# Performance work log

Hardware: AMD Instinct MI355X
Metric: run time of the kernel (lower is better)

## Reference

```python
import jax, jax.numpy as jnp
import numpy as np

B, T, D, H = 8, 512, 768, 768
LN_EPS = 1e-3  # keras LayerNormalization default epsilon


def setup_inputs() -> dict:
    key = jax.random.key(0)
    ks = jax.random.split(key, 16)
    s = 1.0 / np.sqrt(D)  # glorot-ish scale for weight matrices
    return {
        'x': jax.random.normal(ks[0], (B, T, D), jnp.float32),
        'ln1_g': jnp.ones((D,), jnp.float32),
        'ln1_b': jnp.zeros((D,), jnp.float32),
        'ln2_g': jnp.ones((D,), jnp.float32),
        'ln2_b': jnp.zeros((D,), jnp.float32),
        'tm_mix_k': jax.random.uniform(ks[1], (D,), jnp.float32, 0.0, 2.0 / D),
        'tm_mix_v': jax.random.uniform(ks[2], (D,), jnp.float32, 0.0, 2.0 / D),
        'tm_mix_r': jax.random.uniform(ks[3], (D,), jnp.float32, 0.0, (2.0 / D) ** 0.5),
        'tm_key_w': jax.random.normal(ks[4], (D, H), jnp.float32) * s,
        'tm_value_w': jax.random.normal(ks[5], (D, H), jnp.float32) * s,
        'tm_rec_w': jax.random.normal(ks[6], (D, H), jnp.float32) * s,
        'time_decay': jax.random.uniform(ks[7], (H,), jnp.float32, 0.0, 1.0),
        'time_first': jax.random.uniform(ks[8], (H,), jnp.float32, 0.0, 0.05),
        'out_w': jax.random.normal(ks[9], (H, D), jnp.float32) * s,
        'cm_mix_k': jax.random.uniform(ks[10], (D,), jnp.float32, 0.0, 2.0 / D),
        'cm_mix_r': jax.random.uniform(ks[11], (D,), jnp.float32, 0.0, 2.0 / D),
        'cm_key_w': jax.random.normal(ks[12], (D, 4 * H), jnp.float32) * s,
        'cm_value_w': jax.random.normal(ks[13], (4 * H, D), jnp.float32) * (0.5 * s),
        'cm_rec_w': jax.random.normal(ks[14], (D, D), jnp.float32) * s,
    }


def _layernorm(z, g, b):
    m = jnp.mean(z, axis=-1, keepdims=True)
    v = jnp.var(z, axis=-1, keepdims=True)
    return (z - m) * jax.lax.rsqrt(v + LN_EPS) * g + b


def reference(x, ln1_g, ln1_b, ln2_g, ln2_b, tm_mix_k, tm_mix_v, tm_mix_r,
              tm_key_w, tm_value_w, tm_rec_w, time_decay, time_first, out_w,
              cm_mix_k, cm_mix_r, cm_key_w, cm_value_w, cm_rec_w):
    # x: [B, T, D]. Sequential RWKV WKV recurrence over T via lax.scan.
    def step(carry, x_t):
        s_cm, s_tm, num, den, q = carry  # [B,D],[B,D],[B,H],[B,H],[B,H]
        # ---- time mixing on ln_1(x_t) ----
        xi = _layernorm(x_t, ln1_g, ln1_b)
        xk = xi * tm_mix_k + s_tm * (1.0 - tm_mix_k)
        xv = xi * tm_mix_v + s_tm * (1.0 - tm_mix_v)
        xr = xi * tm_mix_r + s_tm * (1.0 - tm_mix_r)
        k = xk @ tm_key_w                      # [B,H]
        v = xv @ tm_value_w                    # [B,H]
        sr = jax.nn.sigmoid(xr @ tm_rec_w)     # [B,H]
        # max-stabilized wkv readout
        w = time_first + k
        qq = jnp.maximum(q, w)
        e1 = jnp.exp(q - qq)
        e2 = jnp.exp(w - qq)
        wkv = (e1 * num + e2 * v) / (e1 * den + e2)
        # state update with decay
        w2 = q - jnp.exp(time_decay)
        q_new = jnp.maximum(w2, k)
        e1 = jnp.exp(w2 - q_new)
        e2 = jnp.exp(k - q_new)
        num_new = e1 * num + e2 * v
        den_new = e1 * den + e2
        y = x_t + (sr * wkv) @ out_w
        # ---- channel mixing on ln_2(y) ----
        xc = _layernorm(y, ln2_g, ln2_b)
        xk2 = xc * cm_mix_k + s_cm * (1.0 - cm_mix_k)
        xr2 = xc * cm_mix_r + s_cm * (1.0 - cm_mix_r)
        kv = jnp.square(jax.nn.relu(xk2 @ cm_key_w)) @ cm_value_w
        y = y + jax.nn.sigmoid(xr2 @ cm_rec_w) * kv
        return (xc, xi, num_new, den_new, q_new), y

    b = x.shape[0]
    d = tm_key_w.shape[0]
    h = tm_key_w.shape[1]
    zD = jnp.zeros((b, d), x.dtype)
    zH = jnp.zeros((b, h), x.dtype)
    init = (zD, zD, zH, zH, zH)
    _, ys = jax.lax.scan(step, init, jnp.swapaxes(x, 0, 1))  # ys: [T,B,D]
    return jnp.swapaxes(ys, 0, 1)
```

## Files before the change

### kernel.cpp

```cpp
#include <hip/hip_runtime.h>
#include <cstdint>
#include <cstddef>

#define B_ 8
#define T_ 512
#define D_ 768
#define H_ 768
#define BT_ 4096
#define LN_EPS 1e-3f

typedef short bf16x8 __attribute__((ext_vector_type(8)));
typedef float f32x4 __attribute__((ext_vector_type(4)));

__device__ __forceinline__ ushort f2bf(float f) {
    union { float f; unsigned u; } x; x.f = f;
    unsigned r = (x.u + 0x7FFFu + ((x.u >> 16) & 1u)) >> 16;
    return (ushort)r;
}
__device__ __forceinline__ float bf2f(ushort u) {
    union { unsigned u; float f; } x; x.u = ((unsigned)u) << 16;
    return x.f;
}

#define GLOAD_LDS16(gp, lp)                                                        \
    __builtin_amdgcn_global_load_lds((const __attribute__((address_space(1))) void*)(gp), \
                                     (__attribute__((address_space(3))) void*)(lp), 16, 0, 0)

struct PrepArgs {
    const float *x, *g, *b, *mk, *mv, *mr;
    ushort *xk, *xv, *xr;
    const float* ws[7];
    ushort* wd[7];
};

__global__ __launch_bounds__(256) void prep(PrepArgs a) {
    __shared__ float tl[32][33];
    __shared__ float red[4][4];
    int bid = blockIdx.x;
    const int tid = threadIdx.x;
    if (bid < BT_) {
        const int row = bid;
        const int t = row & (T_ - 1);
        const float* xc = a.x + (size_t)row * D_;
        const float* xp = a.x + (size_t)(row - 1) * D_;
        const float c0 = xc[tid], c1 = xc[tid + 256], c2 = xc[tid + 512];
        float p0 = 0.f, p1 = 0.f, p2 = 0.f;
        if (t > 0) { p0 = xp[tid]; p1 = xp[tid + 256]; p2 = xp[tid + 512]; }
        float sc = c0 + c1 + c2, qc = c0 * c0 + c1 * c1 + c2 * c2;
        float sp = p0 + p1 + p2, qp = p0 * p0 + p1 * p1 + p2 * p2;
        #pragma unroll
        for (int off = 32; off > 0; off >>= 1) {
            sc += __shfl_down(sc, off); qc += __shfl_down(qc, off);
            sp += __shfl_down(sp, off); qp += __shfl_down(qp, off);
        }
        const int wid = tid >> 6;
        if ((tid & 63) == 0) { red[wid][0] = sc; red[wid][1] = qc; red[wid][2] = sp; red[wid][3] = qp; }
        __syncthreads();
        sc = red[0][0] + red[1][0] + red[2][0] + red[3][0];
        qc = red[0][1] + red[1][1] + red[2][1] + red[3][1];
        sp = red[0][2] + red[1][2] + red[2][2] + red[3][2];
        qp = red[0][3] + red[1][3] + red[2][3] + red[3][3];
        const float mc = sc * (1.0f / D_);
        const float rc = rsqrtf(qc * (1.0f / D_) - mc * mc + LN_EPS);
        const float mp = sp * (1.0f / D_);
        const float rp = rsqrtf(qp * (1.0f / D_) - mp * mp + LN_EPS);
        const size_t base = (size_t)row * D_;
        const float cv[3] = {c0, c1, c2};
        const float pv[3] = {p0, p1, p2};
        #pragma unroll
        for (int s = 0; s < 3; ++s) {
            const int d = tid + s * 256;
            const float cn = (cv[s] - mc) * rc * a.g[d] + a.b[d];
            const float pn = (t > 0) ? ((pv[s] - mp) * rp * a.g[d] + a.b[d]) : 0.0f;
            float m;
            m = a.mk[d]; a.xk[base + d] = f2bf(cn * m + pn * (1.f - m));
            m = a.mv[d]; a.xv[base + d] = f2bf(cn * m + pn * (1.f - m));
            m = a.mr[d]; a.xr[base + d] = f2bf(cn * m + pn * (1.f - m));
        }
        return;
    }
    bid -= BT_;
    int z, K, N, n0, k0;
    if (bid < 2880) {
        z = bid / 576; const int i = bid % 576;
        K = 768; N = 768; n0 = (i % 24) * 32; k0 = (i / 24) * 32;
    } else if (bid < 2880 + 2304) {
        z = 5; const int i = bid - 2880;
        K = 768; N = 3072; n0 = (i % 96) * 32; k0 = (i / 96) * 32;
    } else {
        z = 6; const int i = bid - 2880 - 2304;
        K = 3072; N = 768; n0 = (i % 24) * 32; k0 = (i / 24) * 32;
    }
    const float* W = a.ws[z];
    ushort* WT = a.wd[z];
    const int tx = tid & 31, ty = tid >> 5;
    #pragma unroll
    for (int i = 0; i < 4; ++i)
        tl[ty + i * 8][tx] = W[(size_t)(k0 + ty + i * 8) * N + n0 + tx];
    __syncthreads();
    #pragma unroll
    for (int i = 0; i < 4; ++i)
        WT[(size_t)(n0 + ty + i * 8) * K + k0 + tx] = f2bf(tl[tx][ty + i * 8]);
}

__global__ __launch_bounds__(256) void ln_cmix(const float* __restrict__ in,
                                               ushort* __restrict__ xk2,
                                               ushort* __restrict__ xr2,
                                               const float* __restrict__ g,
                                               const float* __restrict__ b,
                                               const float* __restrict__ mk,
                                               const float* __restrict__ mr) {
    const int row = blockIdx.x;
    const int t = row & (T_ - 1);
    const float* xc = in + (size_t)row * D_;
    const float* xp = in + (size_t)(row - 1) * D_;
    const int tid = threadIdx.x;
    const float c0 = xc[tid], c1 = xc[tid + 256], c2 = xc[tid + 512];
    float p0 = 0.f, p1 = 0.f, p2 = 0.f;
    if (t > 0) { p0 = xp[tid]; p1 = xp[tid + 256]; p2 = xp[tid + 512]; }
    float sc = c0 + c1 + c2, qc = c0 * c0 + c1 * c1 + c2 * c2;
    float sp = p0 + p1 + p2, qp = p0 * p0 + p1 * p1 + p2 * p2;
    #pragma unroll
    for (int off = 32; off > 0; off >>= 1) {
        sc += __shfl_down(sc, off); qc += __shfl_down(qc, off);
        sp += __shfl_down(sp, off); qp += __shfl_down(qp, off);
    }
    __shared__ float red[4][4];
    const int wid = tid >> 6;
    if ((tid & 63) == 0) { red[wid][0] = sc; red[wid][1] = qc; red[wid][2] = sp; red[wid][3] = qp; }
    __syncthreads();
    sc = red[0][0] + red[1][0] + red[2][0] + red[3][0];
    qc = red[0][1] + red[1][1] + red[2][1] + red[3][1];
    sp = red[0][2] + red[1][2] + red[2][2] + red[3][2];
    qp = red[0][3] + red[1][3] + red[2][3] + red[3][3];
    const float mc = sc * (1.0f / D_);
    const float rc = rsqrtf(qc * (1.0f / D_) - mc * mc + LN_EPS);
    const float mp = sp * (1.0f / D_);
    const float rp = rsqrtf(qp * (1.0f / D_) - mp * mp + LN_EPS);
    const size_t base = (size_t)row * D_;
    const float cv[3] = {c0, c1, c2};
    const float pv[3] = {p0, p1, p2};
    #pragma unroll
    for (int s = 0; s < 3; ++s) {
        const int d = tid + s * 256;
        const float cn = (cv[s] - mc) * rc * g[d] + b[d];
        const float pn = (t > 0) ? ((pv[s] - mp) * rp * g[d] + b[d]) : 0.0f;
        float m;
        m = mk[d]; xk2[base + d] = f2bf(cn * m + pn * (1.f - m));
        m = mr[d]; xr2[base + d] = f2bf(cn * m + pn * (1.f - m));
    }
}

#define WKV_CH 16
#define WKV_NC 16
#define WKV_L  32

__global__ __launch_bounds__(256) void wkv_scan(const ushort* __restrict__ k,
                                                const ushort* __restrict__ v,
                                                const ushort* __restrict__ srr,
                                                const float* __restrict__ time_decay,
                                                const float* __restrict__ time_first,
                                                ushort* __restrict__ rv) {
    const int c   = threadIdx.x & (WKV_CH - 1);
    const int ch  = threadIdx.x >> 4;
    const int gch = blockIdx.x * WKV_CH + c;
    const int b = gch / H_;
    const int h = gch % H_;
    const float ed = expf(time_decay[h]);
    const float tf = time_first[h];
    const size_t base = (size_t)b * T_ * H_ + h;

    float n = 0.f, d = 0.f, m = -1e30f;
    size_t idx = base + (size_t)(ch * WKV_L) * H_;
    #pragma unroll 4
    for (int t = 0; t < WKV_L; ++t, idx += H_) {
        const float kk = bf2f(k[idx]), vv = bf2f(v[idx]);
        const float w2 = m - ed;
        const float qn = fmaxf(w2, kk);
        const float e1 = expf(w2 - qn), e2 = expf(kk - qn);
        n = e1 * n + e2 * vv;
        d = e1 * d + e2;
        m = qn;
    }

    __shared__ float sn[WKV_NC][WKV_CH], sd[WKV_NC][WKV_CH], sm[WKV_NC][WKV_CH];
    sn[ch][c] = n; sd[ch][c] = d; sm[ch][c] = m;
    __syncthreads();

    if (ch == 0) {
        float pn = 0.f, pd = 0.f, pm = -1e30f;
        #pragma unroll
        for (int j = 0; j < WKV_NC; ++j) {
            const float nn = sn[j][c], dd = sd[j][c], m2 = sm[j][c];
            sn[j][c] = pn; sd[j][c] = pd; sm[j][c] = pm;
            const float w2 = pm - ed * (float)WKV_L;
            const float mm = fmaxf(w2, m2);
            const float e1 = expf(w2 - mm), e2 = expf(m2 - mm);
            pn = e1 * pn + e2 * nn;
            pd = e1 * pd + e2 * dd;
            pm = mm;
        }
    }
    __syncthreads();

    n = sn[ch][c]; d = sd[ch][c]; m = sm[ch][c];
    idx = base + (size_t)(ch * WKV_L) * H_;
    #pragma unroll 4
    for (int t = 0; t < WKV_L; ++t, idx += H_) {
        const float kk = bf2f(k[idx]), vv = bf2f(v[idx]), ss = bf2f(srr[idx]);
        const float w  = tf + kk;
        const float qq = fmaxf(m, w);
        const float e1 = expf(m - qq), e2 = expf(w - qq);
        const float wkvv = (e1 * n + e2 * vv) / (e1 * d + e2);
        rv[idx] = f2bf(ss * wkvv);
        const float w2 = m - ed;
        const float qn = fmaxf(w2, kk);
        const float a  = expf(w2 - qn), bb = expf(kk - qn);
        n = a * n + bb * vv;
        d = a * d + bb;
        m = qn;
    }
}

template <int BM, int NF>
__device__ __forceinline__ void run_gemm(const ushort* __restrict__ A,
                                         const ushort* __restrict__ Bt,
                                         int K, int bm, int bn,
                                         ushort* As, ushort* Bs,
                                         f32x4 (&acc)[BM / 32][NF], int t) {
    constexpr int MF = BM / 32;
    constexpr int BN = NF * 32;
    constexpr int ASTRIDE = BM * 64;
    constexpr int BSTRIDE = BN * 64;
    const int l = t & 63, wid = t >> 6;
    const int wr = wid >> 1, wc = wid & 1;
    const int lr = l & 15, lg = l >> 4;
    const int l8 = l >> 3, j8 = l & 7;
    const int gcol = ((j8 ^ l8) << 3);
    const int rsw = lr & 7;

    auto STAGE = [&](int buf, int k0) {
        #pragma unroll
        for (int p = 0; p < MF; ++p) {
            const int r = wid * (BM / 4) + p * 8 + l8;
            GLOAD_LDS16(A + (size_t)(bm + r) * K + k0 + gcol,
                        As + buf * ASTRIDE + (wid * (BM / 4) + p * 8) * 64);
        }
        #pragma unroll
        for (int p = 0; p < NF; ++p) {
            const int r = wid * (BN / 4) + p * 8 + l8;
            GLOAD_LDS16(Bt + (size_t)(bn + r) * K + k0 + gcol,
                        Bs + buf * BSTRIDE + (wid * (BN / 4) + p * 8) * 64);
        }
    };

    STAGE(0, 0);
    const int nt = K >> 6;
    int cur = 0;
    for (int it = 0; it < nt; ++it) {
        if (it + 1 < nt) {
            STAGE(cur ^ 1, (it + 1) << 6);
            constexpr int VC = MF + NF;
            if constexpr (VC == 4)      asm volatile("s_waitcnt vmcnt(4)" ::: "memory");
            else if constexpr (VC == 5) asm volatile("s_waitcnt vmcnt(5)" ::: "memory");
            else if constexpr (VC == 6) asm volatile("s_waitcnt vmcnt(6)" ::: "memory");
            else                        asm volatile("s_waitcnt vmcnt(8)" ::: "memory");
        } else {
            asm volatile("s_waitcnt vmcnt(0)" ::: "memory");
        }
        __builtin_amdgcn_sched_barrier(0);
        __builtin_amdgcn_s_barrier();
        const ushort* Ab = As + cur * ASTRIDE;
        const ushort* Bb = Bs + cur * BSTRIDE;
        #pragma unroll
        for (int ks = 0; ks < 2; ++ks) {
            const int cidx = ((ks * 4 + lg) ^ rsw) << 3;
            bf16x8 af[MF], bfr[NF];
            #pragma unroll
            for (int mf = 0; mf < MF; ++mf)
                af[mf] = *(const bf16x8*)(Ab + (wr * (BM / 2) + mf * 16 + lr) * 64 + cidx);
            #pragma unroll
            for (int nf = 0; nf < NF; ++nf)
                bfr[nf] = *(const bf16x8*)(Bb + (wc * (BN / 2) + nf * 16 + lr) * 64 + cidx);
            #pragma unroll
            for (int mf = 0; mf < MF; ++mf)
                #pragma unroll
                for (int nf = 0; nf < NF; ++nf)
                    acc[mf][nf] = __builtin_amdgcn_mfma_f32_16x16x32_bf16(
                        af[mf], bfr[nf], acc[mf][nf], 0, 0, 0);
        }
        __builtin_amdgcn_s_barrier();
        cur ^= 1;
    }
}

template <int BM, int NF>
__device__ __forceinline__ void run_gemm3(const ushort* __restrict__ A,
                                          const ushort* __restrict__ Bt,
                                          int K, int bm, int bn,
                                          ushort* As, ushort* Bs,
                                          f32x4 (&acc)[BM / 32][NF], int t) {
    constexpr int MF = BM / 32;
    constexpr int BN = NF * 32;
    constexpr int ASTRIDE = BM * 64;
    constexpr int BSTRIDE = BN * 64;
    const int l = t & 63, wid = t >> 6;
    const int wr = wid >> 1, wc = wid & 1;
    const int lr = l & 15, lg = l >> 4;
    const int l8 = l >> 3, j8 = l & 7;
    const int gcol = ((j8 ^ l8) << 3);
    const int rsw = lr & 7;

    auto STAGE = [&](int buf, int k0) {
        #pragma unroll
        for (int p = 0; p < MF; ++p) {
            GLOAD_LDS16(A + (size_t)(bm + wid * (BM / 4) + p * 8 + l8) * K + k0 + gcol,
                        As + buf * ASTRIDE + (wid * (BM / 4) + p * 8) * 64);
        }
        #pragma unroll
        for (int p = 0; p < NF; ++p) {
            GLOAD_LDS16(Bt + (size_t)(bn + wid * (BN / 4) + p * 8 + l8) * K + k0 + gcol,
                        Bs + buf * BSTRIDE + (wid * (BN / 4) + p * 8) * 64);
        }
    };

    const int nt = K >> 6;
    STAGE(0, 0);
    STAGE(1, 64);
    int cur = 0;
    for (int it = 0; it < nt; ++it) {
        if (it + 2 < nt) {
            int nb = cur + 2; if (nb >= 3) nb -= 3;
            STAGE(nb, (it + 2) << 6);
            constexpr int VC2 = 2 * (MF + NF);
            if constexpr (VC2 == 8)       asm volatile("s_waitcnt vmcnt(8)" ::: "memory");
            else if constexpr (VC2 == 12) asm volatile("s_waitcnt vmcnt(12)" ::: "memory");
            else                          asm volatile("s_waitcnt vmcnt(16)" ::: "memory");
        } else if (it + 1 < nt) {
            constexpr int VC = MF + NF;
            if constexpr (VC == 4)      asm volatile("s_waitcnt vmcnt(4)" ::: "memory");
            else if constexpr (VC == 6) asm volatile("s_waitcnt vmcnt(6)" ::: "memory");
            else                        asm volatile("s_waitcnt vmcnt(8)" ::: "memory");
        } else {
            asm volatile("s_waitcnt vmcnt(0)" ::: "memory");
        }
        __builtin_amdgcn_sched_barrier(0);
        __builtin_amdgcn_s_barrier();
        const ushort* Ab = As + cur * ASTRIDE;
        const ushort* Bb = Bs + cur * BSTRIDE;
        #pragma unroll
        for (int ks = 0; ks < 2; ++ks) {
            const int cidx = ((ks * 4 + lg) ^ rsw) << 3;
            bf16x8 af[MF], bfr[NF];
            #pragma unroll
            for (int mf = 0; mf < MF; ++mf)
                af[mf] = *(const bf16x8*)(Ab + (wr * (BM / 2) + mf * 16 + lr) * 64 + cidx);
            #pragma unroll
            for (int nf = 0; nf < NF; ++nf)
                bfr[nf] = *(const bf16x8*)(Bb + (wc * (BN / 2) + nf * 16 + lr) * 64 + cidx);
            #pragma unroll
            for (int mf = 0; mf < MF; ++mf)
                #pragma unroll
                for (int nf = 0; nf < NF; ++nf)
                    acc[mf][nf] = __builtin_amdgcn_mfma_f32_16x16x32_bf16(
                        af[mf], bfr[nf], acc[mf][nf], 0, 0, 0);
        }
        __builtin_amdgcn_s_barrier();
        cur += 1; if (cur >= 3) cur -= 3;
    }
}

enum { EPI_KVR = 0, EPI_ADDX = 1, EPI_RELU2 = 2 };

template <int EPI, int BM, int BN>
__global__ __launch_bounds__(256) void hgemm(const ushort* __restrict__ Abase,
                                             const ushort* __restrict__ Wbase,
                                             void* __restrict__ Cbase,
                                             const float* __restrict__ aux1,
                                             int M, int N, int K) {
    constexpr int NF = BN / 32;
    constexpr int MF = BM / 32;
    __shared__ ushort As[2 * BM * 64];
    __shared__ ushort Bs[2 * BN * 64];
    const int t = threadIdx.x;
    int lin = blockIdx.y * gridDim.x + blockIdx.x;
    const int q = (gridDim.x * gridDim.y) >> 3;
    lin = (lin & 7) * q + (lin >> 3);
    const int bn = (lin % gridDim.x) * BN;
    const int bm = (lin / gridDim.x) * BM;
    const int z = blockIdx.z;

    const ushort* A  = Abase;
    const ushort* Bt = Wbase;
    float*  Cf = (float*)Cbase;
    ushort* Cu = (ushort*)Cbase;
    if (EPI == EPI_KVR) {
        A  += (size_t)z * ((size_t)M * K);
        Bt += (size_t)z * ((size_t)N * K);
        Cu += (size_t)z * ((size_t)M * N);
    }

    f32x4 acc[MF][NF];
    #pragma unroll
    for (int i = 0; i < MF; ++i)
        #pragma unroll
        for (int j = 0; j < NF; ++j) acc[i][j] = (f32x4){0.f, 0.f, 0.f, 0.f};

    run_gemm<BM, NF>(A, Bt, K, bm, bn, As, Bs, acc, t);

    const int l = t & 63, wid = t >> 6;
    const int wr = wid >> 1, wc = wid & 1;
    const int lr = l & 15, lg = l >> 4;
    #pragma unroll
    for (int mf = 0; mf < MF; ++mf) {
        #pragma unroll
        for (int nf = 0; nf < NF; ++nf) {
            const f32x4 a = acc[mf][nf];
            #pragma unroll
            for (int j = 0; j < 4; ++j) {
                const int row = bm + wr * (BM / 2) + mf * 16 + lg * 4 + j;
                const int col = bn + wc * (BN / 2) + nf * 16 + lr;
                const size_t idx = (size_t)row * N + col;
                const float vacc = a[j];
                if (EPI == EPI_KVR) {
                    Cu[idx] = f2bf((z == 2) ? 1.0f / (1.0f + expf(-vacc)) : vacc);
                } else if (EPI == EPI_ADDX) {
                    Cf[idx] = aux1[idx] + vacc;
                } else {
                    const float r = fmaxf(vacc, 0.0f);
                    Cu[idx] = f2bf(r * r);
                }
            }
        }
    }
}

__global__ __launch_bounds__(256) void kv_sigmul(const ushort* __restrict__ h1,
                                                 const ushort* __restrict__ wtCV,
                                                 const ushort* __restrict__ xr2,
                                                 const ushort* __restrict__ wtCR,
                                                 const float* __restrict__ ymid,
                                                 float* __restrict__ out) {
    __shared__ ushort As[3 * 64 * 64];
    __shared__ ushort Bs[3 * 64 * 64];
    const int t = threadIdx.x;
    int lin = blockIdx.y * gridDim.x + blockIdx.x;
    const int q = (gridDim.x * gridDim.y) >> 3;
    lin = (lin & 7) * q + (lin >> 3);
    const int bn = (lin % gridDim.x) * 64;
    const int bm = (lin / gridDim.x) * 64;

    f32x4 acc1[2][2], acc2[2][2];
    #pragma unroll
    for (int i = 0; i < 2; ++i)
        #pragma unroll
        for (int j = 0; j < 2; ++j) {
            acc1[i][j] = (f32x4){0.f, 0.f, 0.f, 0.f};
            acc2[i][j] = (f32x4){0.f, 0.f, 0.f, 0.f};
        }

    run_gemm3<64, 2>(h1, wtCV, 3072, bm, bn, As, Bs, acc1, t);
    run_gemm3<64, 2>(xr2, wtCR, 768, bm, bn, As, Bs, acc2, t);

    const int l = t & 63, wid = t >> 6;
    const int wr = wid >> 1, wc = wid & 1;
    const int lr = l & 15, lg = l >> 4;
    #pragma unroll
    for (int mf = 0; mf < 2; ++mf) {
        #pragma unroll
        for (int nf = 0; nf < 2; ++nf) {
            #pragma unroll
            for (int j = 0; j < 4; ++j) {
                const int row = bm + wr * 32 + mf * 16 + lg * 4 + j;
                const int col = bn + wc * 32 + nf * 16 + lr;
                const size_t idx = (size_t)row * D_ + col;
                const float sig = 1.0f / (1.0f + expf(-acc2[mf][nf][j]));
                out[idx] = ymid[idx] + sig * acc1[mf][nf][j];
            }
        }
    }
}

extern "C" void kernel_launch(void* const* d_in, const int* in_sizes, int n_in,
                              void* d_out, int out_size, void* d_ws, size_t ws_size,
                              hipStream_t stream) {
    const float* x          = (const float*)d_in[0];
    const float* ln1_g      = (const float*)d_in[1];
    const float* ln1_b      = (const float*)d_in[2];
    const float* ln2_g      = (const float*)d_in[3];
    const float* ln2_b      = (const float*)d_in[4];
    const float* tm_mix_k   = (const float*)d_in[5];
    const float* tm_mix_v   = (const float*)d_in[6];
    const float* tm_mix_r   = (const float*)d_in[7];
    const float* tm_key_w   = (const float*)d_in[8];
    const float* tm_value_w = (const float*)d_in[9];
    const float* tm_rec_w   = (const float*)d_in[10];
    const float* time_decay = (const float*)d_in[11];
    const float* time_first = (const float*)d_in[12];
    const float* out_w      = (const float*)d_in[13];
    const float* cm_mix_k   = (const float*)d_in[14];
    const float* cm_mix_r   = (const float*)d_in[15];
    const float* cm_key_w   = (const float*)d_in[16];
    const float* cm_value_w = (const float*)d_in[17];
    const float* cm_rec_w   = (const float*)d_in[18];
    float* out = (float*)d_out;

    const size_t SZ = (size_t)BT_ * D_;
    float* wsf = (float*)d_ws;
    float* ymid = wsf;
    ushort* ub = (ushort*)(wsf + SZ);
    ushort* a0 = ub;
    ushort* a1 = ub + SZ;
    ushort* a2 = ub + 2 * SZ;
    ushort* h1 = ub + 3 * SZ;
    ushort* kvsr = ub + 7 * SZ;
    ushort* wt = ub + 10 * SZ;
    const size_t W66  = (size_t)768 * 768;
    const size_t WBIG = (size_t)768 * 3072;
    ushort* wtK  = wt;
    ushort* wtV  = wt + W66;
    ushort* wtR  = wt + 2 * W66;
    ushort* wtO  = wt + 3 * W66;
    ushort* wtCR = wt + 4 * W66;
    ushort* wtCK = wt + 5 * W66;
    ushort* wtCV = wt + 5 * W66 + WBIG;

    PrepArgs pa;
    pa.x = x; pa.g = ln1_g; pa.b = ln1_b;
    pa.mk = tm_mix_k; pa.mv = tm_mix_v; pa.mr = tm_mix_r;
    pa.xk = a0; pa.xv = a1; pa.xr = a2;
    pa.ws[0] = tm_key_w;   pa.wd[0] = wtK;
    pa.ws[1] = tm_value_w; pa.wd[1] = wtV;
    pa.ws[2] = tm_rec_w;   pa.wd[2] = wtR;
    pa.ws[3] = out_w;      pa.wd[3] = wtO;
    pa.ws[4] = cm_rec_w;   pa.wd[4] = wtCR;
    pa.ws[5] = cm_key_w;   pa.wd[5] = wtCK;
    pa.ws[6] = cm_value_w; pa.wd[6] = wtCV;

    prep<<<BT_ + 2880 + 2304 + 2304, 256, 0, stream>>>(pa);
    hgemm<EPI_KVR, 64, 64><<<dim3(12, 64, 3), 256, 0, stream>>>(a0, wtK, kvsr, nullptr, BT_, 768, 768);
    wkv_scan<<<(B_ * H_) / WKV_CH, 256, 0, stream>>>(kvsr, kvsr + SZ, kvsr + 2 * SZ,
                                                     time_decay, time_first, a0);
    hgemm<EPI_ADDX, 64, 64><<<dim3(12, 64), 256, 0, stream>>>(a0, wtO, ymid, x, BT_, 768, 768);
    ln_cmix<<<BT_, 256, 0, stream>>>(ymid, a1, a2, ln2_g, ln2_b, cm_mix_k, cm_mix_r);
    hgemm<EPI_RELU2, 64, 128><<<dim3(24, 64), 256, 0, stream>>>(a1, wtCK, h1, nullptr, BT_, 3072, 768);
    kv_sigmul<<<dim3(12, 64), 256, 0, stream>>>(h1, wtCV, a2, wtCR, ymid, out);
}
```

Measured before the change: 164.5 us.

## Load GEMM B operand directly into registers, bypassing LDS in kv_sigmul

The kv_sigmul GEMM helper now streams only the A tile through LDS with a double buffer, replacing the triple buffer. Each wave loads its B (weight) fragments from global memory straight into registers, two K-steps ahead. This removes the LDS writes and reads for B, halves LDS use per block and may raise occupancy. In exchange the B global loads are 16-byte strided per lane with less coalescing, the loads are duplicated across the two wave rows, and prefetch depth drops from three stages to two.

Result: slower. 219.9 us (+33.7%).

```diff
diff --git a/kernel.cpp b/kernel.cpp
--- a/kernel.cpp
+++ b/kernel.cpp
@@ -295,15 +295,14 @@
 }
 
 template <int BM, int NF>
-__device__ __forceinline__ void run_gemm3(const ushort* __restrict__ A,
-                                          const ushort* __restrict__ Bt,
-                                          int K, int bm, int bn,
-                                          ushort* As, ushort* Bs,
-                                          f32x4 (&acc)[BM / 32][NF], int t) {
+__device__ __forceinline__ void run_gemm_breg(const ushort* __restrict__ A,
+                                              const ushort* __restrict__ Bt,
+                                              int K, int bm, int bn,
+                                              ushort* As,
+                                              f32x4 (&acc)[BM / 32][NF], int t) {
     constexpr int MF = BM / 32;
     constexpr int BN = NF * 32;
     constexpr int ASTRIDE = BM * 64;
-    constexpr int BSTRIDE = BN * 64;
     const int l = t & 63, wid = t >> 6;
     const int wr = wid >> 1, wc = wid & 1;
     const int lr = l & 15, lg = l >> 4;
@@ -311,62 +310,71 @@
     const int gcol = ((j8 ^ l8) << 3);
     const int rsw = lr & 7;
 
-    auto STAGE = [&](int buf, int k0) {
-        #pragma unroll
-        for (int p = 0; p < MF; ++p) {
+    const ushort* Bw = Bt + (size_t)(bn + wc * (BN / 2) + lr) * K + (lg << 3);
+
+    auto STAGE_A = [&](int buf, int k0) {
+        #pragma unroll
+        for (int p = 0; p < MF; ++p)
             GLOAD_LDS16(A + (size_t)(bm + wid * (BM / 4) + p * 8 + l8) * K + k0 + gcol,
                         As + buf * ASTRIDE + (wid * (BM / 4) + p * 8) * 64);
-        }
-        #pragma unroll
-        for (int p = 0; p < NF; ++p) {
-            GLOAD_LDS16(Bt + (size_t)(bn + wid * (BN / 4) + p * 8 + l8) * K + k0 + gcol,
-                        Bs + buf * BSTRIDE + (wid * (BN / 4) + p * 8) * 64);
-        }
     };
 
-    const int nt = K >> 6;
-    STAGE(0, 0);
-    STAGE(1, 64);
-    int cur = 0;
-    for (int it = 0; it < nt; ++it) {
-        if (it + 2 < nt) {
-            int nb = cur + 2; if (nb >= 3) nb -= 3;
-            STAGE(nb, (it + 2) << 6);
-            constexpr int VC2 = 2 * (MF + NF);
-            if constexpr (VC2 == 8)       asm volatile("s_waitcnt vmcnt(8)" ::: "memory");
-            else if constexpr (VC2 == 12) asm volatile("s_waitcnt vmcnt(12)" ::: "memory");
-            else                          asm volatile("s_waitcnt vmcnt(16)" ::: "memory");
-        } else if (it + 1 < nt) {
-            constexpr int VC = MF + NF;
-            if constexpr (VC == 4)      asm volatile("s_waitcnt vmcnt(4)" ::: "memory");
-            else if constexpr (VC == 6) asm volatile("s_waitcnt vmcnt(6)" ::: "memory");
-            else                        asm volatile("s_waitcnt vmcnt(8)" ::: "memory");
-        } else {
-            asm volatile("s_waitcnt vmcnt(0)" ::: "memory");
-        }
-        __builtin_amdgcn_sched_barrier(0);
-        __builtin_amdgcn_s_barrier();
-        const ushort* Ab = As + cur * ASTRIDE;
-        const ushort* Bb = Bs + cur * BSTRIDE;
+    bf16x8 b0[2][NF], b1[2][NF];
+    auto LOADB = [&](bf16x8 (&br)[2][NF], int k0) {
+        #pragma unroll
+        for (int ks = 0; ks < 2; ++ks)
+            #pragma unroll
+            for (int nf = 0; nf < NF; ++nf)
+                br[ks][nf] = *(const bf16x8*)(Bw + (size_t)(nf * 16) * K + k0 + ks * 32);
+    };
+
+    auto MFMAS = [&](const ushort* Ab, bf16x8 (&br)[2][NF]) {
         #pragma unroll
         for (int ks = 0; ks < 2; ++ks) {
             const int cidx = ((ks * 4 + lg) ^ rsw) << 3;
-            bf16x8 af[MF], bfr[NF];
+            bf16x8 af[MF];
             #pragma unroll
             for (int mf = 0; mf < MF; ++mf)
                 af[mf] = *(const bf16x8*)(Ab + (wr * (BM / 2) + mf * 16 + lr) * 64 + cidx);
-            #pragma unroll
-            for (int nf = 0; nf < NF; ++nf)
-                bfr[nf] = *(const bf16x8*)(Bb + (wc * (BN / 2) + nf * 16 + lr) * 64 + cidx);
             #pragma unroll
             for (int mf = 0; mf < MF; ++mf)
                 #pragma unroll
                 for (int nf = 0; nf < NF; ++nf)
                     acc[mf][nf] = __builtin_amdgcn_mfma_f32_16x16x32_bf16(
-                        af[mf], bfr[nf], acc[mf][nf], 0, 0, 0);
-        }
+                        af[mf], br[ks][nf], acc[mf][nf], 0, 0, 0);
+        }
+    };
+
+    constexpr int VC = MF + 2 * NF;
+    const int nt = K >> 6;
+    STAGE_A(0, 0);
+    LOADB(b0, 0);
+    for (int it = 0; it < nt; it += 2) {
+        STAGE_A(1, (it + 1) << 6);
+        LOADB(b1, (it + 1) << 6);
+        if constexpr (VC == 6)       asm volatile("s_waitcnt vmcnt(6)" ::: "memory");
+        else if constexpr (VC == 8)  asm volatile("s_waitcnt vmcnt(8)" ::: "memory");
+        else if constexpr (VC == 10) asm volatile("s_waitcnt vmcnt(10)" ::: "memory");
+        else                         asm volatile("s_waitcnt vmcnt(12)" ::: "memory");
+        __builtin_amdgcn_sched_barrier(0);
         __builtin_amdgcn_s_barrier();
-        cur += 1; if (cur >= 3) cur -= 3;
+        MFMAS(As, b0);
+        __builtin_amdgcn_s_barrier();
+
+        if (it + 2 < nt) {
+            STAGE_A(0, (it + 2) << 6);
+            LOADB(b0, (it + 2) << 6);
+            if constexpr (VC == 6)       asm volatile("s_waitcnt vmcnt(6)" ::: "memory");
+            else if constexpr (VC == 8)  asm volatile("s_waitcnt vmcnt(8)" ::: "memory");
+            else if constexpr (VC == 10) asm volatile("s_waitcnt vmcnt(10)" ::: "memory");
+            else                         asm volatile("s_waitcnt vmcnt(12)" ::: "memory");
+        } else {
+            asm volatile("s_waitcnt vmcnt(0)" ::: "memory");
+        }
+        __builtin_amdgcn_sched_barrier(0);
+        __builtin_amdgcn_s_barrier();
+        MFMAS(As + ASTRIDE, b1);
+        __builtin_amdgcn_s_barrier();
     }
 }
 
@@ -441,8 +449,7 @@
                                                  const ushort* __restrict__ wtCR,
                                                  const float* __restrict__ ymid,
                                                  float* __restrict__ out) {
-    __shared__ ushort As[3 * 64 * 64];
-    __shared__ ushort Bs[3 * 64 * 64];
+    __shared__ ushort As[2 * 64 * 64];
     const int t = threadIdx.x;
     int lin = blockIdx.y * gridDim.x + blockIdx.x;
     const int q = (gridDim.x * gridDim.y) >> 3;
@@ -459,8 +466,8 @@
             acc2[i][j] = (f32x4){0.f, 0.f, 0.f, 0.f};
         }
 
-    run_gemm3<64, 2>(h1, wtCV, 3072, bm, bn, As, Bs, acc1, t);
-    run_gemm3<64, 2>(xr2, wtCR, 768, bm, bn, As, Bs, acc2, t);
+    run_gemm_breg<64, 2>(h1, wtCV, 3072, bm, bn, As, acc1, t);
+    run_gemm_breg<64, 2>(xr2, wtCR, 768, bm, bn, As, acc2, t);
 
     const int l = t & 63, wid = t >> 6;
     const int wr = wid >> 1, wc = wid & 1;
```

## Use single-barrier triple-buffered GEMM mainloop and apply it to BN=64 hgemm

Applied to the files above, without the earlier changes.

Replaces the 3-stage, prefetch-depth-2 GEMM loop with a triple-buffered loop that prefetches one tile ahead and needs only one workgroup barrier per K step. The ring of three buffers makes the trailing barrier unnecessary. The hgemm kernels with BN=64 now use this loop with tripled LDS buffers, and the channel-mix fused kernel gets a __syncthreads between its two GEMMs. This removes a barrier per iteration but cuts the prefetch depth, which may expose more global-load latency. The larger LDS footprint may also lower occupancy.

Result: faster. 160.0 us (-2.7%).

```diff
diff --git a/kernel.cpp b/kernel.cpp
--- a/kernel.cpp
+++ b/kernel.cpp
@@ -295,11 +295,11 @@
 }
 
 template <int BM, int NF>
-__device__ __forceinline__ void run_gemm3(const ushort* __restrict__ A,
-                                          const ushort* __restrict__ Bt,
-                                          int K, int bm, int bn,
-                                          ushort* As, ushort* Bs,
-                                          f32x4 (&acc)[BM / 32][NF], int t) {
+__device__ __forceinline__ void run_gemm_sb(const ushort* __restrict__ A,
+                                            const ushort* __restrict__ Bt,
+                                            int K, int bm, int bn,
+                                            ushort* As, ushort* Bs,
+                                            f32x4 (&acc)[BM / 32][NF], int t) {
     constexpr int MF = BM / 32;
     constexpr int BN = NF * 32;
     constexpr int ASTRIDE = BM * 64;
@@ -314,31 +314,28 @@
     auto STAGE = [&](int buf, int k0) {
         #pragma unroll
         for (int p = 0; p < MF; ++p) {
-            GLOAD_LDS16(A + (size_t)(bm + wid * (BM / 4) + p * 8 + l8) * K + k0 + gcol,
+            const int r = wid * (BM / 4) + p * 8 + l8;
+            GLOAD_LDS16(A + (size_t)(bm + r) * K + k0 + gcol,
                         As + buf * ASTRIDE + (wid * (BM / 4) + p * 8) * 64);
         }
         #pragma unroll
         for (int p = 0; p < NF; ++p) {
-            GLOAD_LDS16(Bt + (size_t)(bn + wid * (BN / 4) + p * 8 + l8) * K + k0 + gcol,
+            const int r = wid * (BN / 4) + p * 8 + l8;
+            GLOAD_LDS16(Bt + (size_t)(bn + r) * K + k0 + gcol,
                         Bs + buf * BSTRIDE + (wid * (BN / 4) + p * 8) * 64);
         }
     };
 
+    STAGE(0, 0);
     const int nt = K >> 6;
-    STAGE(0, 0);
-    STAGE(1, 64);
     int cur = 0;
     for (int it = 0; it < nt; ++it) {
-        if (it + 2 < nt) {
-            int nb = cur + 2; if (nb >= 3) nb -= 3;
-            STAGE(nb, (it + 2) << 6);
-            constexpr int VC2 = 2 * (MF + NF);
-            if constexpr (VC2 == 8)       asm volatile("s_waitcnt vmcnt(8)" ::: "memory");
-            else if constexpr (VC2 == 12) asm volatile("s_waitcnt vmcnt(12)" ::: "memory");
-            else                          asm volatile("s_waitcnt vmcnt(16)" ::: "memory");
-        } else if (it + 1 < nt) {
+        if (it + 1 < nt) {
+            int nb = cur + 1; if (nb == 3) nb = 0;
+            STAGE(nb, (it + 1) << 6);
             constexpr int VC = MF + NF;
             if constexpr (VC == 4)      asm volatile("s_waitcnt vmcnt(4)" ::: "memory");
+            else if constexpr (VC == 5) asm volatile("s_waitcnt vmcnt(5)" ::: "memory");
             else if constexpr (VC == 6) asm volatile("s_waitcnt vmcnt(6)" ::: "memory");
             else                        asm volatile("s_waitcnt vmcnt(8)" ::: "memory");
         } else {
@@ -346,6 +343,7 @@
         }
         __builtin_amdgcn_sched_barrier(0);
         __builtin_amdgcn_s_barrier();
+        __builtin_amdgcn_sched_barrier(0);
         const ushort* Ab = As + cur * ASTRIDE;
         const ushort* Bb = Bs + cur * BSTRIDE;
         #pragma unroll
@@ -365,8 +363,7 @@
                     acc[mf][nf] = __builtin_amdgcn_mfma_f32_16x16x32_bf16(
                         af[mf], bfr[nf], acc[mf][nf], 0, 0, 0);
         }
-        __builtin_amdgcn_s_barrier();
-        cur += 1; if (cur >= 3) cur -= 3;
+        cur += 1; if (cur == 3) cur = 0;
     }
 }
 
@@ -380,8 +377,9 @@
                                              int M, int N, int K) {
     constexpr int NF = BN / 32;
     constexpr int MF = BM / 32;
-    __shared__ ushort As[2 * BM * 64];
-    __shared__ ushort Bs[2 * BN * 64];
+    constexpr bool SB = (BN == 64);
+    __shared__ ushort As[(SB ? 3 : 2) * BM * 64];
+    __shared__ ushort Bs[(SB ? 3 : 2) * BN * 64];
     const int t = threadIdx.x;
     int lin = blockIdx.y * gridDim.x + blockIdx.x;
     const int q = (gridDim.x * gridDim.y) >> 3;
@@ -406,7 +404,10 @@
         #pragma unroll
         for (int j = 0; j < NF; ++j) acc[i][j] = (f32x4){0.f, 0.f, 0.f, 0.f};
 
-    run_gemm<BM, NF>(A, Bt, K, bm, bn, As, Bs, acc, t);
+    if constexpr (SB)
+        run_gemm_sb<BM, NF>(A, Bt, K, bm, bn, As, Bs, acc, t);
+    else
+        run_gemm<BM, NF>(A, Bt, K, bm, bn, As, Bs, acc, t);
 
     const int l = t & 63, wid = t >> 6;
     const int wr = wid >> 1, wc = wid & 1;
@@ -459,8 +460,9 @@
             acc2[i][j] = (f32x4){0.f, 0.f, 0.f, 0.f};
         }
 
-    run_gemm3<64, 2>(h1, wtCV, 3072, bm, bn, As, Bs, acc1, t);
-    run_gemm3<64, 2>(xr2, wtCR, 768, bm, bn, As, Bs, acc2, t);
+    run_gemm_sb<64, 2>(h1, wtCV, 3072, bm, bn, As, Bs, acc1, t);
+    __syncthreads();
+    run_gemm_sb<64, 2>(xr2, wtCR, 768, bm, bn, As, Bs, acc2, t);
 
     const int l = t & 63, wid = t >> 6;
     const int wr = wid >> 1, wc = wid & 1;
```
